# Kernel optimization log

Hardware: AMD Instinct MI355X
Metric: run time of the kernel (lower is better)

The kernel has to match this reference:

```python
import jax, jax.numpy as jnp
import numpy as np

D_MODEL = 1024
NUM_HEADS = 16
DEPTH = D_MODEL // NUM_HEADS


def setup_inputs() -> dict:
    key = jax.random.key(0)
    ks = jax.random.split(key, 11)
    B, S, D = 2, 2048, D_MODEL
    s = 1.0 / np.sqrt(D)
    inp = {
        'x': jax.random.normal(ks[0], (B, S, D), jnp.float32),
        'pH': jax.random.normal(ks[1], (B, 1, 1), jnp.float32),
        'Wq': jax.random.normal(ks[2], (D, D), jnp.float32) * s,
        'bq': jnp.zeros((D,), jnp.float32),
        'Wk': jax.random.normal(ks[3], (D, D), jnp.float32) * s,
        'bk': jnp.zeros((D,), jnp.float32),
        'Wv': jax.random.normal(ks[4], (D, D), jnp.float32) * s,
        'bv': jnp.zeros((D,), jnp.float32),
        'Wo': jax.random.normal(ks[5], (D, D), jnp.float32) * s,
        'bo': jnp.zeros((D,), jnp.float32),
    }
    return inp


def reference(x, pH, Wq, bq, Wk, bk, Wv, bv, Wo, bo):
    B, S, D = x.shape
    H, dh = NUM_HEADS, DEPTH
    # QKV projections -> [B, H, S, dh]
    def proj(W, b):
        return (x @ W + b).reshape(B, S, H, dh).transpose(0, 2, 1, 3)
    q = proj(Wq, bq)
    k = proj(Wk, bk)
    v = proj(Wv, bv)
    # scores [B, H, S, S] with additive per-sample pH bias broadcast over heads/positions
    scores = jnp.einsum('bhqd,bhkd->bhqk', q, k) / jnp.sqrt(jnp.asarray(dh, x.dtype))
    scores = scores + pH[:, :, :, None]  # [B,1,1,1] broadcasts to [B,H,S,S]
    attn = jax.nn.softmax(scores, axis=-1)
    out = jnp.einsum('bhqk,bhkd->bhqd', attn, v)  # [B,H,S,dh]
    out = out.transpose(0, 2, 1, 3).reshape(B, S, D)
    return out @ Wo + bo  # dropout p=0.0 -> identity
```

## Files before the change

### kernel.cpp

```cpp
#include <hip/hip_runtime.h>
#include <hip/hip_bf16.h>
#include <math.h>

#define BATCH 2
#define SEQ   2048
#define DMODEL 1024
#define NHEADS 16
#define DHEAD 64
#define MROWS (BATCH*SEQ)

typedef __attribute__((ext_vector_type(8))) short bf16x8;
typedef __attribute__((ext_vector_type(4))) short bf16x4;
typedef __attribute__((ext_vector_type(4))) float f32x4;

__device__ __forceinline__ short f2bf(float f) {
    union { float f; unsigned u; } c; c.f = f;
    unsigned r = (c.u + 0x7fffu + ((c.u >> 16) & 1u)) >> 16;
    return (short)r;
}
__device__ __forceinline__ float truncmask(unsigned u) {
    union { unsigned u; float f; } c; c.u = u & 0xffff0000u;
    return c.f;
}

__device__ __forceinline__ void async_ld16(const void* g, void* l) {
    __builtin_amdgcn_global_load_lds(
        (const __attribute__((address_space(1))) unsigned*)g,
        (__attribute__((address_space(3))) unsigned*)l, 16, 0, 0);
}

__global__ __launch_bounds__(256) void convert_h(
    const float* __restrict__ in, short* __restrict__ hi, int n8)
{
    const int i = blockIdx.x * 256 + threadIdx.x;
    if (i >= n8) return;
    const float4* p = (const float4*)in + (size_t)i * 2;
    float4 a = p[0], b = p[1];
    float v[8] = {a.x, a.y, a.z, a.w, b.x, b.y, b.z, b.w};
    bf16x8 H;
    #pragma unroll
    for (int j = 0; j < 8; ++j) H[j] = f2bf(v[j]);
    *((bf16x8*)hi + i) = H;
}

__global__ __launch_bounds__(256) void transpose_w4(
    const float* __restrict__ W0, const float* __restrict__ W1,
    const float* __restrict__ W2, const float* __restrict__ W3,
    short* __restrict__ oqkv, short* __restrict__ oo)
{
    __shared__ float T[64][65];
    const int tid = threadIdx.x;
    const int z = blockIdx.z;
    const float* W = (z == 0) ? W0 : (z == 1) ? W1 : (z == 2) ? W2 : W3;
    short* out = (z < 3) ? (oqkv + (size_t)z * 1024 * 1024) : oo;
    const int n0 = blockIdx.x * 64, k0 = blockIdx.y * 64;
    #pragma unroll
    for (int i = 0; i < 16; ++i) {
        const int idx = tid + i * 256;
        const int r = idx >> 6, c = idx & 63;
        T[r][c] = W[(size_t)(k0 + r) * DMODEL + n0 + c];
    }
    __syncthreads();
    #pragma unroll
    for (int i = 0; i < 4; ++i) {
        const int idx = tid + i * 256;
        const int r = idx >> 4, g = idx & 15;
        bf16x4 H;
        #pragma unroll
        for (int j = 0; j < 4; ++j)
            H[j] = f2bf(T[g * 4 + j][r]);
        *(bf16x4*)(out + (size_t)(n0 + r) * DMODEL + k0 + g * 4) = H;
    }
}

#define GBK 64

__global__ __launch_bounds__(256) void mfma_gemm(
    const short* __restrict__ Ahi, const short* __restrict__ Bthi,
    const float* __restrict__ b0, const float* __restrict__ b1, const float* __restrict__ b2,
    short* __restrict__ oqh, short* __restrict__ okh, short* __restrict__ ovh,
    float* __restrict__ outf, int mode, float qscale)
{
    __shared__ short Ah[128 * GBK], Bh[128 * GBK];

    const int tid  = threadIdx.x;
    const int lane = tid & 63;
    const int w    = tid >> 6;
    const int quad = lane >> 4;
    const int l15  = lane & 15;
    const int wr   = w >> 1, wc = w & 1;
    const int m0   = blockIdx.y * 128;
    const int n0   = blockIdx.x * 128;
    const int K    = DMODEL;

    f32x4 acc[4][4] = {};

    int srow[4], spos[4];
    #pragma unroll
    for (int j = 0; j < 4; ++j) {
        const int c = w * 256 + j * 64 + lane;
        srow[j] = c >> 3;
        spos[j] = (c & 7) ^ (srow[j] & 7);
    }

    for (int k0 = 0; k0 < K; k0 += GBK) {
        __syncthreads();
        #pragma unroll
        for (int j = 0; j < 4; ++j) {
            const int cB = (w * 256 + j * 64) * 8;
            async_ld16(Ahi + (size_t)(m0 + srow[j]) * K + k0 + spos[j] * 8, Ah + cB);
            async_ld16(Bthi + (size_t)(n0 + srow[j]) * K + k0 + spos[j] * 8, Bh + cB);
        }
        __syncthreads();

        #pragma unroll
        for (int s = 0; s < 2; ++s) {
            bf16x8 afh[4], bfh[4];
            #pragma unroll
            for (int mi = 0; mi < 4; ++mi) {
                const int row = wr * 64 + mi * 16 + l15;
                const int pos = (s * 4 + quad) ^ (row & 7);
                afh[mi] = *(const bf16x8*)(Ah + row * GBK + pos * 8);
            }
            #pragma unroll
            for (int ni = 0; ni < 4; ++ni) {
                const int row = wc * 64 + ni * 16 + l15;
                const int pos = (s * 4 + quad) ^ (row & 7);
                bfh[ni] = *(const bf16x8*)(Bh + row * GBK + pos * 8);
            }
            #pragma unroll
            for (int mi = 0; mi < 4; ++mi)
                #pragma unroll
                for (int ni = 0; ni < 4; ++ni)
                    acc[mi][ni] = __builtin_amdgcn_mfma_f32_16x16x32_bf16(
                        afh[mi], bfh[ni], acc[mi][ni], 0, 0, 0);
        }
    }

    const int nbase = n0 + wc * 64;
    if (mode == 1) {
        #pragma unroll
        for (int mi = 0; mi < 4; ++mi)
            #pragma unroll
            for (int ni = 0; ni < 4; ++ni)
                #pragma unroll
                for (int r = 0; r < 4; ++r) {
                    const int m = m0 + wr * 64 + mi * 16 + quad * 4 + r;
                    const int nn = nbase + ni * 16 + l15;
                    outf[(size_t)m * DMODEL + nn] = acc[mi][ni][r] + b0[nn];
                }
    } else {
        const int which = nbase >> 10;
        if (which < 2) {
            const float* bias = which ? b1 : b0;
            short* dst = which ? okh : oqh;
            const float scl = which ? 1.0f : qscale;
            #pragma unroll
            for (int mi = 0; mi < 4; ++mi)
                #pragma unroll
                for (int ni = 0; ni < 4; ++ni)
                    #pragma unroll
                    for (int r = 0; r < 4; ++r) {
                        const int m = m0 + wr * 64 + mi * 16 + quad * 4 + r;
                        const int nn = (nbase + ni * 16 + l15) & 1023;
                        const int b = m >> 11, s = m & (SEQ - 1);
                        const int h = nn >> 6, d = nn & 63;
                        dst[((size_t)(b * NHEADS + h) * SEQ + s) * DHEAD + d] =
                            f2bf((acc[mi][ni][r] + bias[nn]) * scl);
                    }
        } else {
            #pragma unroll
            for (int mi = 0; mi < 4; ++mi) {
                const int mb = m0 + wr * 64 + mi * 16 + quad * 4;
                const int b = mb >> 11, s0 = mb & (SEQ - 1);
                #pragma unroll
                for (int ni = 0; ni < 4; ++ni) {
                    const int nn = (nbase + ni * 16 + l15) & 1023;
                    const int h = nn >> 6, d = nn & 63;
                    bf16x4 H;
                    #pragma unroll
                    for (int r = 0; r < 4; ++r)
                        H[r] = f2bf(acc[mi][ni][r] + b2[nn]);
                    *(bf16x4*)(ovh + ((size_t)(b * NHEADS + h) * DHEAD + d) * SEQ + s0) = H;
                }
            }
        }
    }
}

#define PP 72

__global__ __launch_bounds__(256) void attn_mfma(
    const short* __restrict__ Qh_g, const short* __restrict__ Kh_g,
    const short* __restrict__ Vth_g, short* __restrict__ Oh_g)
{
    __shared__ short Ksh[4096];
    __shared__ short Vsh[4096];
    __shared__ short Ph[4][16 * PP];

    const int tid  = threadIdx.x;
    const int lane = tid & 63;
    const int w    = tid >> 6;
    const int quad = lane >> 4;
    const int l15  = lane & 15;

    const int bh    = blockIdx.x & 31;
    const int qtile = blockIdx.x >> 5;
    const int q0    = qtile * 64 + w * 16;
    const size_t kvb = (size_t)bh * SEQ * DHEAD;

    bf16x8 qhi[2];
    {
        const size_t qr = kvb + (size_t)(q0 + l15) * DHEAD;
        qhi[0] = *(const bf16x8*)(Qh_g + qr + quad * 8);
        qhi[1] = *(const bf16x8*)(Qh_g + qr + 32 + quad * 8);
    }

    short* dst = (w < 2) ? Ksh : Vsh;
    const bool isv = (w >= 2);
    int srow[4], spos[4];
    #pragma unroll
    for (int j = 0; j < 4; ++j) {
        const int c = (w & 1) * 256 + j * 64 + lane;
        srow[j] = c >> 3;
        spos[j] = (c & 7) ^ (srow[j] & 7);
    }

    f32x4 o[4] = {};
    float l_run = 0.f;

    for (int kb = 0; kb < SEQ; kb += 64) {
        __syncthreads();
        {
            const short* src = isv ? (Vth_g + kvb + kb) : (Kh_g + kvb + (size_t)kb * DHEAD);
            #pragma unroll
            for (int j = 0; j < 4; ++j) {
                const short* g = src + (isv ? ((size_t)srow[j] * SEQ + spos[j] * 8)
                                            : ((size_t)srow[j] * DHEAD + spos[j] * 8));
                async_ld16(g, dst + ((w & 1) * 256 + j * 64) * 8);
            }
        }
        __syncthreads();

        #pragma unroll
        for (int mf = 0; mf < 4; ++mf) {
            const int row = mf * 16 + l15;
            const int sw = row & 7;
            bf16x8 kh0 = *(const bf16x8*)(Ksh + row * 64 + ((quad ^ sw) * 8));
            bf16x8 kh1 = *(const bf16x8*)(Ksh + row * 64 + (((4 + quad) ^ sw) * 8));
            f32x4 c = {};
            c = __builtin_amdgcn_mfma_f32_16x16x32_bf16(kh0, qhi[0], c, 0, 0, 0);
            c = __builtin_amdgcn_mfma_f32_16x16x32_bf16(kh1, qhi[1], c, 0, 0, 0);

            unsigned u[4];
            #pragma unroll
            for (int r = 0; r < 4; ++r) {
                union { float f; unsigned u; } p;
                p.f = __builtin_amdgcn_exp2f(c[r]);
                u[r] = p.u;
                l_run += truncmask(u[r]);
            }
            const unsigned pk01 = __builtin_amdgcn_perm(u[1], u[0], 0x07060302u);
            const unsigned pk23 = __builtin_amdgcn_perm(u[3], u[2], 0x07060302u);
            uint2 pk; pk.x = pk01; pk.y = pk23;
            *(uint2*)(&Ph[w][l15 * PP + mf * 16 + quad * 4]) = pk;
        }

        bf16x8 ph0 = *(const bf16x8*)(&Ph[w][l15 * PP + quad * 8]);
        bf16x8 ph1 = *(const bf16x8*)(&Ph[w][l15 * PP + 32 + quad * 8]);

        #pragma unroll
        for (int nf = 0; nf < 4; ++nf) {
            const int row = nf * 16 + l15;
            const int sw = row & 7;
            bf16x8 vh0 = *(const bf16x8*)(Vsh + row * 64 + ((quad ^ sw) * 8));
            bf16x8 vh1 = *(const bf16x8*)(Vsh + row * 64 + (((4 + quad) ^ sw) * 8));
            f32x4 c = o[nf];
            c = __builtin_amdgcn_mfma_f32_16x16x32_bf16(ph0, vh0, c, 0, 0, 0);
            c = __builtin_amdgcn_mfma_f32_16x16x32_bf16(ph1, vh1, c, 0, 0, 0);
            o[nf] = c;
        }
    }

    float ls = l_run;
    ls += __shfl_xor(ls, 16, 64);
    ls += __shfl_xor(ls, 32, 64);
    float li[4];
    #pragma unroll
    for (int r = 0; r < 4; ++r)
        li[r] = 1.0f / __shfl(ls, quad * 4 + r, 64);

    const int b = bh >> 4, hh = bh & 15;
    #pragma unroll
    for (int nf = 0; nf < 4; ++nf) {
        #pragma unroll
        for (int r = 0; r < 4; ++r) {
            const int q = q0 + quad * 4 + r;
            const int d = nf * 16 + l15;
            Oh_g[(size_t)(b * SEQ + q) * DMODEL + hh * DHEAD + d] = f2bf(o[nf][r] * li[r]);
        }
    }
}

extern "C" void kernel_launch(void* const* d_in, const int* in_sizes, int n_in,
                              void* d_out, int out_size, void* d_ws, size_t ws_size,
                              hipStream_t stream) {
    const float* x  = (const float*)d_in[0];
    const float* Wq = (const float*)d_in[2];
    const float* bq = (const float*)d_in[3];
    const float* Wk = (const float*)d_in[4];
    const float* bk = (const float*)d_in[5];
    const float* Wv = (const float*)d_in[6];
    const float* bv = (const float*)d_in[7];
    const float* Wo = (const float*)d_in[8];
    const float* bo = (const float*)d_in[9];
    float* out = (float*)d_out;

    char* ws = (char*)d_ws;
    const size_t MB = 1024 * 1024;
    short* qh  = (short*)(ws + 0 * MB);
    short* kh  = (short*)(ws + 16 * MB);
    short* vth = (short*)(ws + 32 * MB);
    short* aoh = (short*)(ws + 48 * MB);
    short* xhi = (short*)(ws + 64 * MB);
    short* wqkv_hi = (short*)(ws + 80 * MB);
    short* wto_hi  = (short*)(ws + 92 * MB);

    dim3 blk(256);
    const int n8 = MROWS * DMODEL / 8;

    hipLaunchKernelGGL(convert_h, dim3(n8 / 256), blk, 0, stream, x, xhi, n8);
    hipLaunchKernelGGL(transpose_w4, dim3(16, 16, 4), blk, 0, stream,
                       Wq, Wk, Wv, Wo, wqkv_hi, wto_hi);

    const float qscale = 0.125f * 1.44269504088896f;
    hipLaunchKernelGGL(mfma_gemm, dim3(3072 / 128, MROWS / 128), blk, 0, stream,
                       xhi, wqkv_hi, bq, bk, bv,
                       qh, kh, vth, (float*)nullptr, 0, qscale);

    hipLaunchKernelGGL(attn_mfma, dim3(BATCH * NHEADS * (SEQ / 64)), blk, 0, stream,
                       qh, kh, vth, aoh);

    hipLaunchKernelGGL(mfma_gemm, dim3(1024 / 128, MROWS / 128), blk, 0, stream,
                       aoh, wto_hi, bo, bo, bo,
                       (short*)nullptr, (short*)nullptr, (short*)nullptr,
                       out, 1, 1.0f);
}
```

Baseline: 216.6 us.

## Stage QKV GEMM epilogue through LDS and double attention query rows per wave

Measured after the change: 210.4 us. 2.9% less time.

```diff
diff --git a/kernel.cpp b/kernel.cpp
--- a/kernel.cpp
+++ b/kernel.cpp
@@ -150,10 +150,16 @@
                     outf[(size_t)m * DMODEL + nn] = acc[mi][ni][r] + b0[nn];
                 }
     } else {
+        __syncthreads();
+        short* scr = (w < 2) ? (Ah + w * 4096) : (Bh + (w - 2) * 4096);
         const int which = nbase >> 10;
+        const int hh = (nbase & 1023) >> 6;
+        const int mb = m0 + wr * 64;
+        const int b = mb >> 11, sbase = mb & (SEQ - 1);
+
         if (which < 2) {
             const float* bias = which ? b1 : b0;
-            short* dst = which ? okh : oqh;
+            short* dstp = which ? okh : oqh;
             const float scl = which ? 1.0f : qscale;
             #pragma unroll
             for (int mi = 0; mi < 4; ++mi)
@@ -161,28 +167,40 @@
                 for (int ni = 0; ni < 4; ++ni)
                     #pragma unroll
                     for (int r = 0; r < 4; ++r) {
-                        const int m = m0 + wr * 64 + mi * 16 + quad * 4 + r;
+                        const int sloc = mi * 16 + quad * 4 + r;
+                        const int dloc = ni * 16 + l15;
                         const int nn = (nbase + ni * 16 + l15) & 1023;
-                        const int b = m >> 11, s = m & (SEQ - 1);
-                        const int h = nn >> 6, d = nn & 63;
-                        dst[((size_t)(b * NHEADS + h) * SEQ + s) * DHEAD + d] =
+                        scr[sloc * 64 + (((dloc >> 3) ^ (sloc & 7)) * 8) + (dloc & 7)] =
                             f2bf((acc[mi][ni][r] + bias[nn]) * scl);
                     }
+            #pragma unroll
+            for (int i = 0; i < 8; ++i) {
+                const int sloc = i * 8 + (lane >> 3);
+                const int cph = (lane & 7) ^ (sloc & 7);
+                bf16x8 row = *(const bf16x8*)(scr + sloc * 64 + cph * 8);
+                const int dloc = (lane & 7) * 8;
+                *(bf16x8*)(dstp + ((size_t)(b * NHEADS + hh) * SEQ + sbase + sloc) * DHEAD + dloc) = row;
+            }
         } else {
             #pragma unroll
-            for (int mi = 0; mi < 4; ++mi) {
-                const int mb = m0 + wr * 64 + mi * 16 + quad * 4;
-                const int b = mb >> 11, s0 = mb & (SEQ - 1);
+            for (int mi = 0; mi < 4; ++mi)
                 #pragma unroll
-                for (int ni = 0; ni < 4; ++ni) {
-                    const int nn = (nbase + ni * 16 + l15) & 1023;
-                    const int h = nn >> 6, d = nn & 63;
-                    bf16x4 H;
+                for (int ni = 0; ni < 4; ++ni)
                     #pragma unroll
-                    for (int r = 0; r < 4; ++r)
-                        H[r] = f2bf(acc[mi][ni][r] + b2[nn]);
-                    *(bf16x4*)(ovh + ((size_t)(b * NHEADS + h) * DHEAD + d) * SEQ + s0) = H;
-                }
+                    for (int r = 0; r < 4; ++r) {
+                        const int sloc = mi * 16 + quad * 4 + r;
+                        const int dloc = ni * 16 + l15;
+                        const int nn = (nbase + ni * 16 + l15) & 1023;
+                        scr[dloc * 64 + (((sloc >> 3) ^ (dloc & 7)) * 8) + (sloc & 7)] =
+                            f2bf(acc[mi][ni][r] + b2[nn]);
+                    }
+            #pragma unroll
+            for (int i = 0; i < 8; ++i) {
+                const int dloc = i * 8 + (lane >> 3);
+                const int cph = (lane & 7) ^ (dloc & 7);
+                bf16x8 row = *(const bf16x8*)(scr + dloc * 64 + cph * 8);
+                const int sg = sbase + (lane & 7) * 8;
+                *(bf16x8*)(ovh + ((size_t)(b * NHEADS + hh) * DHEAD + dloc) * SEQ + sg) = row;
             }
         }
     }
@@ -196,7 +214,7 @@
 {
     __shared__ short Ksh[4096];
     __shared__ short Vsh[4096];
-    __shared__ short Ph[4][16 * PP];
+    __shared__ short Ph[4][2][16 * PP];
 
     const int tid  = threadIdx.x;
     const int lane = tid & 63;
@@ -206,14 +224,17 @@
 
     const int bh    = blockIdx.x & 31;
     const int qtile = blockIdx.x >> 5;
-    const int q0    = qtile * 64 + w * 16;
+    const int q0    = qtile * 128 + w * 32;
     const size_t kvb = (size_t)bh * SEQ * DHEAD;
 
-    bf16x8 qhi[2];
+    bf16x8 qA[2], qB[2];
     {
-        const size_t qr = kvb + (size_t)(q0 + l15) * DHEAD;
-        qhi[0] = *(const bf16x8*)(Qh_g + qr + quad * 8);
-        qhi[1] = *(const bf16x8*)(Qh_g + qr + 32 + quad * 8);
+        const size_t qrA = kvb + (size_t)(q0 + l15) * DHEAD;
+        const size_t qrB = kvb + (size_t)(q0 + 16 + l15) * DHEAD;
+        qA[0] = *(const bf16x8*)(Qh_g + qrA + quad * 8);
+        qA[1] = *(const bf16x8*)(Qh_g + qrA + 32 + quad * 8);
+        qB[0] = *(const bf16x8*)(Qh_g + qrB + quad * 8);
+        qB[1] = *(const bf16x8*)(Qh_g + qrB + 32 + quad * 8);
     }
 
     short* dst = (w < 2) ? Ksh : Vsh;
@@ -226,8 +247,8 @@
         spos[j] = (c & 7) ^ (srow[j] & 7);
     }
 
-    f32x4 o[4] = {};
-    float l_run = 0.f;
+    f32x4 oA[4] = {}, oB[4] = {};
+    float lA = 0.f, lB = 0.f;
 
     for (int kb = 0; kb < SEQ; kb += 64) {
         __syncthreads();
@@ -248,26 +269,34 @@
             const int sw = row & 7;
             bf16x8 kh0 = *(const bf16x8*)(Ksh + row * 64 + ((quad ^ sw) * 8));
             bf16x8 kh1 = *(const bf16x8*)(Ksh + row * 64 + (((4 + quad) ^ sw) * 8));
-            f32x4 c = {};
-            c = __builtin_amdgcn_mfma_f32_16x16x32_bf16(kh0, qhi[0], c, 0, 0, 0);
-            c = __builtin_amdgcn_mfma_f32_16x16x32_bf16(kh1, qhi[1], c, 0, 0, 0);
-
-            unsigned u[4];
+            f32x4 cA = {}, cB = {};
+            cA = __builtin_amdgcn_mfma_f32_16x16x32_bf16(kh0, qA[0], cA, 0, 0, 0);
+            cA = __builtin_amdgcn_mfma_f32_16x16x32_bf16(kh1, qA[1], cA, 0, 0, 0);
+            cB = __builtin_amdgcn_mfma_f32_16x16x32_bf16(kh0, qB[0], cB, 0, 0, 0);
+            cB = __builtin_amdgcn_mfma_f32_16x16x32_bf16(kh1, qB[1], cB, 0, 0, 0);
+
+            unsigned uA[4], uB[4];
             #pragma unroll
             for (int r = 0; r < 4; ++r) {
                 union { float f; unsigned u; } p;
-                p.f = __builtin_amdgcn_exp2f(c[r]);
-                u[r] = p.u;
-                l_run += truncmask(u[r]);
-            }
-            const unsigned pk01 = __builtin_amdgcn_perm(u[1], u[0], 0x07060302u);
-            const unsigned pk23 = __builtin_amdgcn_perm(u[3], u[2], 0x07060302u);
-            uint2 pk; pk.x = pk01; pk.y = pk23;
-            *(uint2*)(&Ph[w][l15 * PP + mf * 16 + quad * 4]) = pk;
-        }
-
-        bf16x8 ph0 = *(const bf16x8*)(&Ph[w][l15 * PP + quad * 8]);
-        bf16x8 ph1 = *(const bf16x8*)(&Ph[w][l15 * PP + 32 + quad * 8]);
+                p.f = __builtin_amdgcn_exp2f(cA[r]);
+                uA[r] = p.u; lA += truncmask(uA[r]);
+                p.f = __builtin_amdgcn_exp2f(cB[r]);
+                uB[r] = p.u; lB += truncmask(uB[r]);
+            }
+            uint2 pkA, pkB;
+            pkA.x = __builtin_amdgcn_perm(uA[1], uA[0], 0x07060302u);
+            pkA.y = __builtin_amdgcn_perm(uA[3], uA[2], 0x07060302u);
+            pkB.x = __builtin_amdgcn_perm(uB[1], uB[0], 0x07060302u);
+            pkB.y = __builtin_amdgcn_perm(uB[3], uB[2], 0x07060302u);
+            *(uint2*)(&Ph[w][0][l15 * PP + mf * 16 + quad * 4]) = pkA;
+            *(uint2*)(&Ph[w][1][l15 * PP + mf * 16 + quad * 4]) = pkB;
+        }
+
+        bf16x8 pA0 = *(const bf16x8*)(&Ph[w][0][l15 * PP + quad * 8]);
+        bf16x8 pA1 = *(const bf16x8*)(&Ph[w][0][l15 * PP + 32 + quad * 8]);
+        bf16x8 pB0 = *(const bf16x8*)(&Ph[w][1][l15 * PP + quad * 8]);
+        bf16x8 pB1 = *(const bf16x8*)(&Ph[w][1][l15 * PP + 32 + quad * 8]);
 
         #pragma unroll
         for (int nf = 0; nf < 4; ++nf) {
@@ -275,29 +304,34 @@
             const int sw = row & 7;
             bf16x8 vh0 = *(const bf16x8*)(Vsh + row * 64 + ((quad ^ sw) * 8));
             bf16x8 vh1 = *(const bf16x8*)(Vsh + row * 64 + (((4 + quad) ^ sw) * 8));
-            f32x4 c = o[nf];
-            c = __builtin_amdgcn_mfma_f32_16x16x32_bf16(ph0, vh0, c, 0, 0, 0);
-            c = __builtin_amdgcn_mfma_f32_16x16x32_bf16(ph1, vh1, c, 0, 0, 0);
-            o[nf] = c;
-        }
-    }
-
-    float ls = l_run;
-    ls += __shfl_xor(ls, 16, 64);
-    ls += __shfl_xor(ls, 32, 64);
-    float li[4];
-    #pragma unroll
-    for (int r = 0; r < 4; ++r)
-        li[r] = 1.0f / __shfl(ls, quad * 4 + r, 64);
+            f32x4 cA = oA[nf], cB = oB[nf];
+            cA = __builtin_amdgcn_mfma_f32_16x16x32_bf16(pA0, vh0, cA, 0, 0, 0);
+            cA = __builtin_amdgcn_mfma_f32_16x16x32_bf16(pA1, vh1, cA, 0, 0, 0);
+            cB = __builtin_amdgcn_mfma_f32_16x16x32_bf16(pB0, vh0, cB, 0, 0, 0);
+            cB = __builtin_amdgcn_mfma_f32_16x16x32_bf16(pB1, vh1, cB, 0, 0, 0);
+            oA[nf] = cA; oB[nf] = cB;
+        }
+    }
+
+    float lsA = lA, lsB = lB;
+    lsA += __shfl_xor(lsA, 16, 64);  lsA += __shfl_xor(lsA, 32, 64);
+    lsB += __shfl_xor(lsB, 16, 64);  lsB += __shfl_xor(lsB, 32, 64);
+    float liA[4], liB[4];
+    #pragma unroll
+    for (int r = 0; r < 4; ++r) {
+        liA[r] = 1.0f / __shfl(lsA, quad * 4 + r, 64);
+        liB[r] = 1.0f / __shfl(lsB, quad * 4 + r, 64);
+    }
 
     const int b = bh >> 4, hh = bh & 15;
     #pragma unroll
     for (int nf = 0; nf < 4; ++nf) {
         #pragma unroll
         for (int r = 0; r < 4; ++r) {
-            const int q = q0 + quad * 4 + r;
+            const int qa = q0 + quad * 4 + r;
             const int d = nf * 16 + l15;
-            Oh_g[(size_t)(b * SEQ + q) * DMODEL + hh * DHEAD + d] = f2bf(o[nf][r] * li[r]);
+            Oh_g[(size_t)(b * SEQ + qa) * DMODEL + hh * DHEAD + d] = f2bf(oA[nf][r] * liA[r]);
+            Oh_g[(size_t)(b * SEQ + qa + 16) * DMODEL + hh * DHEAD + d] = f2bf(oB[nf][r] * liB[r]);
         }
     }
 }
@@ -338,7 +372,7 @@
                        xhi, wqkv_hi, bq, bk, bv,
                        qh, kh, vth, (float*)nullptr, 0, qscale);
 
-    hipLaunchKernelGGL(attn_mfma, dim3(BATCH * NHEADS * (SEQ / 64)), blk, 0, stream,
+    hipLaunchKernelGGL(attn_mfma, dim3(BATCH * NHEADS * (SEQ / 128)), blk, 0, stream,
                        qh, kh, vth, aoh);
 
     hipLaunchKernelGGL(mfma_gemm, dim3(1024 / 128, MROWS / 128), blk, 0, stream,
```
